# Kernel optimization log

Hardware: AMD Instinct MI355X
Metric: run time of the kernel (lower is better)

## Reference

```python
import jax, jax.numpy as jnp
import numpy as np

N, D, O, H, T, S, R, BN = 4096, 256, 256, 256, 512, 8, 4, 2  # nodes, in, out, hidden, text_len, adj_size, relations used, basis_num


def setup_inputs() -> dict:
    key = jax.random.key(0)
    ks = jax.random.split(key, 16)
    sc = 0.05
    return {
        "entity_embeddings": jax.random.normal(ks[0], (N, D), jnp.float32) * sc,
        "text_encodings": jax.random.normal(ks[1], (1, T, 2 * H), jnp.float32) * sc,
        "adj_to_use": jnp.arange(R, dtype=jnp.int32),
        "adj_masks": jax.random.randint(ks[2], (R, N, N), 0, 2, dtype=jnp.int32),
        "text_guids": jax.random.normal(ks[3], (S, 2 * H), jnp.float32) * sc,
        "graph_guids_1": jax.random.normal(ks[4], (S, D), jnp.float32) * sc,
        "graph_guids_2": jax.random.normal(ks[5], (S, D), jnp.float32) * sc,
        "guid_a": jax.random.normal(ks[6], (S,), jnp.float32),
        "basis_V": jax.random.normal(ks[7], (D, BN, O), jnp.float32) * sc,
        "basis_b": jax.random.normal(ks[8], (S, BN), jnp.float32) * sc,
        "W_1": jax.random.normal(ks[9], (2 * H, D), jnp.float32) * sc,
        "W_2": jax.random.normal(ks[10], (2 * H, D), jnp.float32) * sc,
        "ln_gamma": jnp.ones((O,), jnp.float32),
        "ln_beta": jnp.zeros((O,), jnp.float32),
    }


def reference(entity_embeddings, text_encodings, adj_to_use, adj_masks,
              text_guids, graph_guids_1, graph_guids_2, guid_a,
              basis_V, basis_b, W_1, W_2, ln_gamma, ln_beta):
    te = text_encodings[0]                                  # [T, 2H] (batch of 1)
    tg = text_guids[adj_to_use]                             # [R, 2H]
    # text attention: softmax over T, per relation
    att = jax.nn.softmax(te @ tg.T, axis=0)                 # [T, R]
    context = att.T @ te                                    # [R, 2H]
    c1 = context @ W_1                                      # [R, D]
    c2 = context @ W_2
    ga = jax.nn.sigmoid(guid_a[adj_to_use])[:, None]        # [R, 1]
    g1 = ga * graph_guids_1[adj_to_use] + (1.0 - ga) * c1   # [R, D]
    g2 = ga * graph_guids_2[adj_to_use] + (1.0 - ga) * c2
    s1 = entity_embeddings @ g1.T                           # [N, R]
    s2 = entity_embeddings @ g2.T
    # A[r,i,j] = s1[i,r] + s2[j,r], masked softmax over j
    A = s1.T[:, :, None] + s2.T[:, None, :]                 # [R, N, N]
    A = jnp.where(adj_masks == 1, A, jnp.float32(-1e10))
    A = jax.nn.softmax(A, axis=-1)
    fused = jnp.einsum('rij,jd->rid', A, entity_embeddings) # [R, N, D]
    # torch.cat over relations on last dim -> column index r*D + d
    fused_cat = jnp.transpose(fused, (1, 0, 2)).reshape(N, R * D)
    # torch.matmul([R,BN],[D,BN,O]) -> [D,R,O], then .view(R*D, O) (row index d*R + r)
    bb = basis_b[adj_to_use]                                # [R, BN]
    W = jnp.einsum('rb,dbo->dro', bb, basis_V).reshape(D * R, O)
    out = fused_cat @ W                                     # [N, O]
    mu = jnp.mean(out, axis=-1, keepdims=True)
    var = jnp.var(out, axis=-1, keepdims=True)
    out = (out - mu) / jnp.sqrt(var + 1e-5) * ln_gamma + ln_beta
    return jax.nn.relu(out)
```

## Files before the change

kernel.cpp:

```cpp
#include <hip/hip_runtime.h>
#include <hip/hip_bf16.h>


typedef unsigned short u16;
typedef short bf16x8 __attribute__((ext_vector_type(8)));
typedef float f32x4 __attribute__((ext_vector_type(4)));
typedef int   v4i   __attribute__((ext_vector_type(4)));
typedef unsigned int v2u __attribute__((ext_vector_type(2)));

#define G2_OFF    0
#define E2_OFF    4096
#define WRT_OFF   69632
#define FPT_OFF   593920
#define FUSED_OFF 9506816
#define CAN_OFF   26284032

#define C_ENT 0
#define C_TE  1048576
#define C_TG  1310720
#define C_GG2 1314816
#define C_GA  1316864
#define C_BV  1316872
#define C_BB  1447944
#define C_W2  1447960
#define C_GAM 1579032
#define C_BET 1579288

__device__ __forceinline__ float b2f(u16 u) {
    union { unsigned int i; float f; } v; v.i = ((unsigned int)u) << 16; return v.f;
}
__device__ __forceinline__ u16 f2b(float f) {
    union { float f; unsigned int i; } v; v.f = f;
    return (u16)((v.i + 0x7FFFu + ((v.i >> 16) & 1u)) >> 16);
}

__global__ __launch_bounds__(256) void k_cvt(
    const void* s0, const void* s1, const void* s2, const void* s3,
    const void* s4, const void* s5, const void* s6, const void* s7,
    const void* s8, const void* s9, const unsigned* __restrict__ graw,
    u16* __restrict__ dst)
{
    bool isbf = (graw[0] == 0x3F803F80u);
    const void* srcs[10] = {s0, s1, s2, s3, s4, s5, s6, s7, s8, s9};
    const int ns[10]     = {1048576, 262144, 4096, 2048, 8, 131072, 16, 131072, 256, 256};
    const int offs[10]   = {C_ENT, C_TE, C_TG, C_GG2, C_GA, C_BV, C_BB, C_W2, C_GAM, C_BET};
    const int bstart[11] = {0, 512, 640, 642, 643, 644, 708, 709, 773, 774, 775};
    int b = blockIdx.x, a = 0;
    while (b >= bstart[a + 1]) ++a;
    int rel = b - bstart[a];
    int n = ns[a];
    u16* d = dst + offs[a];
    int base = rel * 2048 + threadIdx.x;
    if (isbf) {
        const u16* s = (const u16*)srcs[a];
        for (int k = 0; k < 8; ++k) { int i = base + k * 256; if (i < n) d[i] = s[i]; }
    } else {
        const float* s = (const float*)srcs[a];
        for (int k = 0; k < 8; ++k) { int i = base + k * 256; if (i < n) d[i] = f2b(s[i]); }
    }
}

__global__ __launch_bounds__(1024) void k_pre(const u16* __restrict__ te,
                                              const int* __restrict__ adj,
                                              const u16* __restrict__ tguids,
                                              const u16* __restrict__ gg2,
                                              const u16* __restrict__ guida,
                                              const u16* __restrict__ W2,
                                              float* __restrict__ g2ws) {
    __shared__ float s_tg[4 * 512];
    __shared__ float s_att[512 * 4];
    __shared__ float s_red[512 * 4];
    __shared__ float s_ctx[4 * 512];
    __shared__ float s_part[1024 * 4];
    int tid = threadIdx.x;
    int a[4] = {adj[0], adj[1], adj[2], adj[3]};
    for (int idx = tid; idx < 2048; idx += 1024) {
        int r = idx >> 9, h = idx & 511;
        s_tg[r * 512 + h] = b2f(tguids[a[r] * 512 + h]);
    }
    __syncthreads();
    {
        int t = tid & 511, half = tid >> 9;
        int h0 = half * 256;
        float s0 = 0.f, s1 = 0.f, s2 = 0.f, s3 = 0.f;
        const u16* row = te + t * 512 + h0;
        for (int hb = 0; hb < 256; hb += 8) {
            bf16x8 v = *(const bf16x8*)(row + hb);
            #pragma unroll
            for (int k = 0; k < 8; ++k) {
                float tv = b2f((u16)v[k]);
                int h = h0 + hb + k;
                s0 += tv * s_tg[h];        s1 += tv * s_tg[512 + h];
                s2 += tv * s_tg[1024 + h]; s3 += tv * s_tg[1536 + h];
            }
        }
        s_part[tid * 4 + 0] = s0; s_part[tid * 4 + 1] = s1;
        s_part[tid * 4 + 2] = s2; s_part[tid * 4 + 3] = s3;
    }
    __syncthreads();
    if (tid < 512) {
        for (int r = 0; r < 4; ++r) {
            float s = s_part[tid * 4 + r] + s_part[(512 + tid) * 4 + r];
            s_att[tid * 4 + r] = s; s_red[tid * 4 + r] = s;
        }
    }
    __syncthreads();
    for (int st = 256; st > 0; st >>= 1) {
        if (tid < st) for (int r = 0; r < 4; ++r)
            s_red[tid * 4 + r] = fmaxf(s_red[tid * 4 + r], s_red[(tid + st) * 4 + r]);
        __syncthreads();
    }
    float mx[4]; for (int r = 0; r < 4; ++r) mx[r] = s_red[r];
    __syncthreads();
    if (tid < 512) for (int r = 0; r < 4; ++r) {
        float e = __expf(s_att[tid * 4 + r] - mx[r]);
        s_att[tid * 4 + r] = e; s_red[tid * 4 + r] = e;
    }
    __syncthreads();
    for (int st = 256; st > 0; st >>= 1) {
        if (tid < st) for (int r = 0; r < 4; ++r)
            s_red[tid * 4 + r] += s_red[(tid + st) * 4 + r];
        __syncthreads();
    }
    float dn[4]; for (int r = 0; r < 4; ++r) dn[r] = s_red[r];
    __syncthreads();
    if (tid < 512) for (int r = 0; r < 4; ++r) s_att[tid * 4 + r] /= dn[r];
    __syncthreads();
    {
        int u = tid >> 2, tq = tid & 3;
        int r = u >> 6, h0 = (u & 63) * 8;
        float acc[8] = {};
        int t0 = tq * 128;
        for (int t = t0; t < t0 + 128; ++t) {
            bf16x8 v = *(const bf16x8*)(te + t * 512 + h0);
            float at = s_att[t * 4 + r];
            #pragma unroll
            for (int k = 0; k < 8; ++k) acc[k] += at * b2f((u16)v[k]);
        }
        #pragma unroll
        for (int k = 0; k < 8; ++k) {
            acc[k] += __shfl_xor(acc[k], 1);
            acc[k] += __shfl_xor(acc[k], 2);
        }
        if (tq == 0) {
            #pragma unroll
            for (int k = 0; k < 8; ++k) s_ctx[r * 512 + h0 + k] = acc[k];
        }
    }
    __syncthreads();
    {
        int r = tid >> 8, d = tid & 255;
        float acc = 0.f;
        for (int h = 0; h < 512; ++h) acc += s_ctx[r * 512 + h] * b2f(W2[h * 256 + d]);
        float gav = 1.f / (1.f + expf(-b2f(guida[a[r]])));
        g2ws[r * 256 + d] = gav * b2f(gg2[a[r] * 256 + d]) + (1.f - gav) * acc;
    }
}

__global__ __launch_bounds__(256) void k_s2_wrt(const u16* __restrict__ entity,
                                                const int* __restrict__ adj,
                                                const u16* __restrict__ basisV,
                                                const u16* __restrict__ basisb,
                                                const float* __restrict__ g2ws,
                                                float* __restrict__ e2ws,
                                                u16* __restrict__ wrt) {
    int b = blockIdx.x, tid = threadIdx.x;
    if (b < 16) {
        __shared__ float sg2[1024];
        for (int i = tid; i < 1024; i += 256) sg2[i] = g2ws[i];
        __syncthreads();
        int j = b * 256 + tid;
        const u16* erow = entity + j * 256;
        float a0 = 0.f, a1 = 0.f, a2 = 0.f, a3 = 0.f;
        for (int d0 = 0; d0 < 256; d0 += 8) {
            bf16x8 v = *(const bf16x8*)(erow + d0);
            #pragma unroll
            for (int k = 0; k < 8; ++k) {
                float ev = b2f((u16)v[k]);
                a0 += ev * sg2[d0 + k];       a1 += ev * sg2[256 + d0 + k];
                a2 += ev * sg2[512 + d0 + k]; a3 += ev * sg2[768 + d0 + k];
            }
        }
        e2ws[j] = expf(a0); e2ws[4096 + j] = expf(a1);
        e2ws[8192 + j] = expf(a2); e2ws[12288 + j] = expf(a3);
    } else {
        int b2 = b - 16; int r = b2 >> 6;
        int c = (b2 & 63) * 4 + (tid >> 6);
        int dq = tid & 63;
        int dbase = dq * 4;
        int a[4] = {adj[0], adj[1], adj[2], adj[3]};
        for (int dd = 0; dd < 4; ++dd) {
            float w = 0.f;
            for (int bi = 0; bi < 2; ++bi)
                w += b2f(basisb[a[dd] * 2 + bi]) * b2f(basisV[((64 * r + dq) * 2 + bi) * 256 + c]);
            wrt[(r * 256 + c) * 256 + dbase + dd] = f2b(w);
        }
    }
}

__global__ __launch_bounds__(256) void k_fplus(const u16* __restrict__ entity,
                                               const u16* __restrict__ wrt,
                                               const float* __restrict__ e2ws,
                                               u16* __restrict__ fpt) {
    int b = blockIdx.x, tid = threadIdx.x;
    if (b < 256) {
        int r = b & 3, ct = (b >> 2) & 3, jt = b >> 4;
        int c0 = ct * 64, j0 = jt * 256;
        __shared__ __align__(16) u16 lw[64 * 264];
        const u16* wr = wrt + (r * 256 + c0) * 256;
        for (int k = 0; k < 8; ++k) {
            int ci = tid + k * 256; int row = ci >> 5, off = (ci & 31) * 8;
            *(v4i*)(&lw[row * 264 + off]) = *(const v4i*)(wr + row * 256 + off);
        }
        __syncthreads();
        int wave = tid >> 6, ln = tid & 15, q = (tid & 63) >> 4;
        f32x4 acc[4][4] = {};
        for (int ks = 0; ks < 8; ++ks) {
            bf16x8 afr[4], bfr[4];
            for (int mt = 0; mt < 4; ++mt)
                afr[mt] = *(const bf16x8*)(&lw[(mt * 16 + ln) * 264 + ks * 32 + q * 8]);
            for (int nt = 0; nt < 4; ++nt) {
                int j = j0 + (wave * 4 + nt) * 16 + ln;
                bfr[nt] = *(const bf16x8*)(entity + j * 256 + ks * 32 + q * 8);
            }
            for (int mt = 0; mt < 4; ++mt)
                for (int nt = 0; nt < 4; ++nt)
                    acc[mt][nt] = __builtin_amdgcn_mfma_f32_16x16x32_bf16(afr[mt], bfr[nt], acc[mt][nt], 0, 0, 0);
        }
        for (int nt = 0; nt < 4; ++nt) {
            int j = j0 + (wave * 4 + nt) * 16 + ln;
            float e2j = e2ws[r * 4096 + j];
            int kt = j >> 5, kk = j & 31;
            u16* dst = fpt + (((size_t)(r * 128 + kt)) * 272 << 5);
            for (int mt = 0; mt < 4; ++mt)
                for (int reg = 0; reg < 4; ++reg) {
                    int c = c0 + mt * 16 + q * 4 + reg;
                    dst[(c << 5) + kk] = f2b(acc[mt][nt][reg] * e2j);
                }
        }
    } else {
        int b2 = b - 256; int r = b2 >> 1, half = b2 & 1;
        const float* e2r = e2ws + r * 4096;
        for (int it = 0; it < 128; ++it) {
            int l = it * 256 + tid;
            int kk = l & 31;
            int c  = 256 + ((l >> 5) & 15);
            int kt = half * 64 + (l >> 9);
            fpt[(((size_t)(r * 128 + kt) * 272 + c) << 5) + kk] =
                (c == 256) ? f2b(e2r[kt * 32 + kk]) : (u16)0;
        }
    }
}

__global__ __launch_bounds__(512) void k_big(const int* __restrict__ masks,
                                             const u16* __restrict__ fpt,
                                             float* __restrict__ fused) {
    __shared__ __align__(16) u16 lm[2][64 * 40];
    __shared__ __align__(16) u16 lf[2][272 * 40];
    __shared__ float lden[64];
    int b = blockIdx.x, tid = threadIdx.x;
    int xcd = b & 7; int r = xcd & 3;
    int it = (b >> 3) + ((xcd >> 2) << 5);
    long i0 = (long)it * 64;
    const int* mbase = masks + ((long)r << 24) + i0 * 4096;
    const u16* fbase = fpt + (size_t)r * 128 * 272 * 32;
    int mrow = tid >> 3, mch = tid & 7;
    int wave = tid >> 6, lane = tid & 63, ln = lane & 15, q = lane >> 4;
    int mg = wave >> 2, ng = wave & 3;

    f32x4 acc[2][4] = {};
    f32x4 accD0 = {}, accD1 = {};

    struct Slot { v4i pm, f0, f1, f2; };
    Slot s0, s1, s2, s3;
    auto load_slot = [&](int kt, Slot& s) {
        s.pm = __builtin_nontemporal_load((const v4i*)(mbase + mrow * 4096 + kt * 32 + mch * 4));
        const u16* su = fbase + (size_t)kt * 8704;
        s.f0 = *(const v4i*)(su + tid * 8);
        s.f1 = *(const v4i*)(su + (tid + 512) * 8);
        if (tid < 64) s.f2 = *(const v4i*)(su + (tid + 1024) * 8);
    };
    auto stage = [&](int par, const Slot& s) {
        {
            unsigned m0 = (unsigned)s.pm.x * 0x3F80u, m1 = (unsigned)s.pm.y * 0x3F80u;
            unsigned m2 = (unsigned)s.pm.z * 0x3F80u, m3 = (unsigned)s.pm.w * 0x3F80u;
            v2u w; w.x = m0 | (m1 << 16); w.y = m2 | (m3 << 16);
            *(v2u*)(&lm[par][mrow * 40 + mch * 4]) = w;
        }
        u16* dst = &lf[par][0];
        *(v4i*)(dst + (tid >> 2) * 40 + (tid & 3) * 8) = s.f0;
        { int ci = tid + 512; *(v4i*)(dst + (ci >> 2) * 40 + (ci & 3) * 8) = s.f1; }
        if (tid < 64) { int ci = tid + 1024; *(v4i*)(dst + (ci >> 2) * 40 + (ci & 3) * 8) = s.f2; }
    };
    auto step = [&](int k, Slot& sM, Slot& sF) {
        const u16* msrc = &lm[k & 1][0];
        const u16* src  = &lf[k & 1][0];
        bf16x8 a0 = *(const bf16x8*)(msrc + (mg * 32 + ln) * 40 + q * 8);
        bf16x8 a1 = *(const bf16x8*)(msrc + (mg * 32 + 16 + ln) * 40 + q * 8);
        if (k + 1 < 128) stage((k + 1) & 1, sF);
        if (k + 4 < 128) load_slot(k + 4, sM);
        #pragma unroll
        for (int nt = 0; nt < 4; ++nt) {
            bf16x8 bf = *(const bf16x8*)(src + ((ng * 4 + nt) * 16 + ln) * 40 + q * 8);
            acc[0][nt] = __builtin_amdgcn_mfma_f32_16x16x32_bf16(a0, bf, acc[0][nt], 0, 0, 0);
            acc[1][nt] = __builtin_amdgcn_mfma_f32_16x16x32_bf16(a1, bf, acc[1][nt], 0, 0, 0);
        }
        if (ng == 3) {
            bf16x8 bf = *(const bf16x8*)(src + (256 + ln) * 40 + q * 8);
            accD0 = __builtin_amdgcn_mfma_f32_16x16x32_bf16(a0, bf, accD0, 0, 0, 0);
            accD1 = __builtin_amdgcn_mfma_f32_16x16x32_bf16(a1, bf, accD1, 0, 0, 0);
        }
        __syncthreads();
    };

    load_slot(0, s0);
    load_slot(1, s1);
    load_slot(2, s2);
    load_slot(3, s3);
    stage(0, s0);
    __syncthreads();
    #pragma unroll 1
    for (int kt = 0; kt < 128; kt += 4) {
        step(kt,     s0, s1);
        step(kt + 1, s1, s2);
        step(kt + 2, s2, s3);
        step(kt + 3, s3, s0);
    }

    if (ng == 3 && ln == 0) {
        #pragma unroll
        for (int reg = 0; reg < 4; ++reg) {
            lden[mg * 32 + q * 4 + reg]      = accD0[reg];
            lden[mg * 32 + 16 + q * 4 + reg] = accD1[reg];
        }
    }
    __syncthreads();
    float* fb = fused + ((long)r * 4096 + i0) * 256;
    #pragma unroll
    for (int mt = 0; mt < 2; ++mt) {
        float rd[4];
        #pragma unroll
        for (int reg = 0; reg < 4; ++reg) rd[reg] = 1.0f / lden[mg * 32 + mt * 16 + q * 4 + reg];
        #pragma unroll
        for (int nt = 0; nt < 4; ++nt) {
            int c = (ng * 4 + nt) * 16 + ln;
            #pragma unroll
            for (int reg = 0; reg < 4; ++reg) {
                int row = mg * 32 + mt * 16 + q * 4 + reg;
                __builtin_nontemporal_store(acc[mt][nt][reg] * rd[reg], fb + row * 256 + c);
            }
        }
    }
}

__global__ __launch_bounds__(256) void k_ln(const float* __restrict__ fused,
                                            const u16* __restrict__ gamma,
                                            const u16* __restrict__ beta,
                                            const unsigned* __restrict__ graw,
                                            void* __restrict__ outraw) {
    __shared__ float part[8];
    int i = blockIdx.x, o = threadIdx.x;
    float x = 0.f;
    for (int r = 0; r < 4; ++r)
        x += __builtin_nontemporal_load(fused + ((long)(r << 12) + i) * 256 + o);
    float s = x;
    #pragma unroll
    for (int st = 32; st > 0; st >>= 1) s += __shfl_xor(s, st);
    int w = o >> 6;
    if ((o & 63) == 0) part[w] = s;
    __syncthreads();
    float mu = (part[0] + part[1] + part[2] + part[3]) * (1.f / 256.f);
    float v = x - mu;
    float qv = v * v;
    #pragma unroll
    for (int st = 32; st > 0; st >>= 1) qv += __shfl_xor(qv, st);
    if ((o & 63) == 0) part[4 + w] = qv;
    __syncthreads();
    float var = (part[4] + part[5] + part[6] + part[7]) * (1.f / 256.f);
    float y = v * rsqrtf(var + 1e-5f) * b2f(gamma[o]) + b2f(beta[o]);
    float res = fmaxf(y, 0.f);
    bool isbf = (graw[0] == 0x3F803F80u);
    if (isbf) ((u16*)outraw)[i * 256 + o] = f2b(res);
    else      ((float*)outraw)[i * 256 + o] = res;
}

extern "C" void kernel_launch(void* const* d_in, const int* in_sizes, int n_in,
                              void* d_out, int out_size, void* d_ws, size_t ws_size,
                              hipStream_t stream) {
    const int* adj   = (const int*)d_in[2];
    const int* masks = (const int*)d_in[3];
    const unsigned* graw = (const unsigned*)d_in[12];
    char* ws = (char*)d_ws;
    float* g2ws = (float*)(ws + G2_OFF);
    float* e2ws = (float*)(ws + E2_OFF);
    u16*   wrt  = (u16*)(ws + WRT_OFF);
    u16*   fpt  = (u16*)(ws + FPT_OFF);
    float* fus  = (float*)(ws + FUSED_OFF);
    u16*   can  = (u16*)(ws + CAN_OFF);

    k_cvt<<<775, 256, 0, stream>>>(d_in[0], d_in[1], d_in[4], d_in[6], d_in[7],
                                   d_in[8], d_in[9], d_in[11], d_in[12], d_in[13],
                                   graw, can);
    const u16* entity = can + C_ENT;
    const u16* te     = can + C_TE;
    const u16* tguids = can + C_TG;
    const u16* gg2    = can + C_GG2;
    const u16* guida  = can + C_GA;
    const u16* basisV = can + C_BV;
    const u16* basisb = can + C_BB;
    const u16* W2     = can + C_W2;
    const u16* gamma  = can + C_GAM;
    const u16* beta   = can + C_BET;

    k_pre<<<1, 1024, 0, stream>>>(te, adj, tguids, gg2, guida, W2, g2ws);
    k_s2_wrt<<<272, 256, 0, stream>>>(entity, adj, basisV, basisb, g2ws, e2ws, wrt);
    k_fplus<<<264, 256, 0, stream>>>(entity, wrt, e2ws, fpt);
    k_big<<<256, 512, 0, stream>>>(masks, fpt, fus);
    k_ln<<<4096, 256, 0, stream>>>(fus, gamma, beta, graw, d_out);
}
```

Baseline: 545.5 us.

## Merge front-end kernels and fold exp(s2) into fplus to cut launches

Replaces the separate conversion, text-attention, and s2/basis-weight kernels with one k_front kernel. It converts only the entity table, builds the basis weights from raw inputs, and runs the attention/context/g2 block in a single 512-thread block. The exp(entity·g2) values are now recomputed inside k_fplus blocks instead of being staged through workspace, and the LN kernel reads gamma/beta raw. This removes two kernel launches and the conversion of unused tensors. In exchange, the single-block g2 path runs serially alongside the conversion blocks, and entity dot products are recomputed redundantly per block.

```diff
diff --git a/kernel.cpp b/kernel.cpp
--- a/kernel.cpp
+++ b/kernel.cpp
@@ -5,27 +5,16 @@
 typedef unsigned short u16;
 typedef short bf16x8 __attribute__((ext_vector_type(8)));
 typedef float f32x4 __attribute__((ext_vector_type(4)));
+typedef float f32x8 __attribute__((ext_vector_type(8)));
 typedef int   v4i   __attribute__((ext_vector_type(4)));
 typedef unsigned int v2u __attribute__((ext_vector_type(2)));
 
 #define G2_OFF    0
-#define E2_OFF    4096
 #define WRT_OFF   69632
 #define FPT_OFF   593920
 #define FUSED_OFF 9506816
 #define CAN_OFF   26284032
 
-#define C_ENT 0
-#define C_TE  1048576
-#define C_TG  1310720
-#define C_GG2 1314816
-#define C_GA  1316864
-#define C_BV  1316872
-#define C_BB  1447944
-#define C_W2  1447960
-#define C_GAM 1579032
-#define C_BET 1579288
-
 __device__ __forceinline__ float b2f(u16 u) {
     union { unsigned int i; float f; } v; v.i = ((unsigned int)u) << 16; return v.f;
 }
@@ -33,76 +22,89 @@
     union { float f; unsigned int i; } v; v.f = f;
     return (u16)((v.i + 0x7FFFu + ((v.i >> 16) & 1u)) >> 16);
 }
-
-__global__ __launch_bounds__(256) void k_cvt(
-    const void* s0, const void* s1, const void* s2, const void* s3,
-    const void* s4, const void* s5, const void* s6, const void* s7,
-    const void* s8, const void* s9, const unsigned* __restrict__ graw,
-    u16* __restrict__ dst)
+__device__ __forceinline__ float rawf(const void* p, bool isbf, int i) {
+    return isbf ? b2f(((const u16*)p)[i]) : ((const float*)p)[i];
+}
+__device__ __forceinline__ f32x8 raw8(const void* p, bool isbf, int i8) {
+    f32x8 o;
+    if (isbf) {
+        bf16x8 v = *(const bf16x8*)((const u16*)p + i8);
+        #pragma unroll
+        for (int k = 0; k < 8; ++k) o[k] = b2f((u16)v[k]);
+    } else {
+        const float* f = (const float*)p + i8;
+        float4 a = *(const float4*)f, b = *(const float4*)(f + 4);
+        o[0] = a.x; o[1] = a.y; o[2] = a.z; o[3] = a.w;
+        o[4] = b.x; o[5] = b.y; o[6] = b.z; o[7] = b.w;
+    }
+    return o;
+}
+
+__global__ __launch_bounds__(512) void k_front(
+    const void* __restrict__ ent_raw, const void* __restrict__ te_raw,
+    const int* __restrict__ adj, const void* __restrict__ tg_raw,
+    const void* __restrict__ gg2_raw, const void* __restrict__ ga_raw,
+    const void* __restrict__ bV_raw, const void* __restrict__ bb_raw,
+    const void* __restrict__ W2_raw, const unsigned* __restrict__ graw,
+    u16* __restrict__ ent_can, float* __restrict__ g2ws, u16* __restrict__ wrt)
 {
     bool isbf = (graw[0] == 0x3F803F80u);
-    const void* srcs[10] = {s0, s1, s2, s3, s4, s5, s6, s7, s8, s9};
-    const int ns[10]     = {1048576, 262144, 4096, 2048, 8, 131072, 16, 131072, 256, 256};
-    const int offs[10]   = {C_ENT, C_TE, C_TG, C_GG2, C_GA, C_BV, C_BB, C_W2, C_GAM, C_BET};
-    const int bstart[11] = {0, 512, 640, 642, 643, 644, 708, 709, 773, 774, 775};
-    int b = blockIdx.x, a = 0;
-    while (b >= bstart[a + 1]) ++a;
-    int rel = b - bstart[a];
-    int n = ns[a];
-    u16* d = dst + offs[a];
-    int base = rel * 2048 + threadIdx.x;
-    if (isbf) {
-        const u16* s = (const u16*)srcs[a];
-        for (int k = 0; k < 8; ++k) { int i = base + k * 256; if (i < n) d[i] = s[i]; }
-    } else {
-        const float* s = (const float*)srcs[a];
-        for (int k = 0; k < 8; ++k) { int i = base + k * 256; if (i < n) d[i] = f2b(s[i]); }
-    }
-}
-
-__global__ __launch_bounds__(1024) void k_pre(const u16* __restrict__ te,
-                                              const int* __restrict__ adj,
-                                              const u16* __restrict__ tguids,
-                                              const u16* __restrict__ gg2,
-                                              const u16* __restrict__ guida,
-                                              const u16* __restrict__ W2,
-                                              float* __restrict__ g2ws) {
+    int b = blockIdx.x, tid = threadIdx.x;
+    if (b < 256) {
+        int base = b * 4096 + tid;
+        if (isbf) {
+            const u16* s = (const u16*)ent_raw;
+            #pragma unroll
+            for (int k = 0; k < 8; ++k) { int i = base + k * 512; ent_can[i] = s[i]; }
+        } else {
+            const float* s = (const float*)ent_raw;
+            #pragma unroll
+            for (int k = 0; k < 8; ++k) { int i = base + k * 512; ent_can[i] = f2b(s[i]); }
+        }
+        return;
+    }
+    if (b < 384) {
+        int b2 = b - 256;
+        int r = b2 >> 5, cq = b2 & 31;
+        int c = cq * 8 + (tid >> 6);
+        int dq = tid & 63;
+        int a[4] = {adj[0], adj[1], adj[2], adj[3]};
+        #pragma unroll
+        for (int dd = 0; dd < 4; ++dd) {
+            float w = 0.f;
+            #pragma unroll
+            for (int bi = 0; bi < 2; ++bi)
+                w += rawf(bb_raw, isbf, a[dd] * 2 + bi) *
+                     rawf(bV_raw, isbf, ((64 * r + dq) * 2 + bi) * 256 + c);
+            wrt[(r * 256 + c) * 256 + dq * 4 + dd] = f2b(w);
+        }
+        return;
+    }
     __shared__ float s_tg[4 * 512];
     __shared__ float s_att[512 * 4];
     __shared__ float s_red[512 * 4];
     __shared__ float s_ctx[4 * 512];
-    __shared__ float s_part[1024 * 4];
-    int tid = threadIdx.x;
     int a[4] = {adj[0], adj[1], adj[2], adj[3]};
-    for (int idx = tid; idx < 2048; idx += 1024) {
+    for (int idx = tid; idx < 2048; idx += 512) {
         int r = idx >> 9, h = idx & 511;
-        s_tg[r * 512 + h] = b2f(tguids[a[r] * 512 + h]);
+        s_tg[r * 512 + h] = rawf(tg_raw, isbf, a[r] * 512 + h);
     }
     __syncthreads();
     {
-        int t = tid & 511, half = tid >> 9;
-        int h0 = half * 256;
         float s0 = 0.f, s1 = 0.f, s2 = 0.f, s3 = 0.f;
-        const u16* row = te + t * 512 + h0;
-        for (int hb = 0; hb < 256; hb += 8) {
-            bf16x8 v = *(const bf16x8*)(row + hb);
+        for (int hb = 0; hb < 512; hb += 8) {
+            f32x8 v = raw8(te_raw, isbf, tid * 512 + hb);
             #pragma unroll
             for (int k = 0; k < 8; ++k) {
-                float tv = b2f((u16)v[k]);
-                int h = h0 + hb + k;
+                float tv = v[k]; int h = hb + k;
                 s0 += tv * s_tg[h];        s1 += tv * s_tg[512 + h];
                 s2 += tv * s_tg[1024 + h]; s3 += tv * s_tg[1536 + h];
             }
         }
-        s_part[tid * 4 + 0] = s0; s_part[tid * 4 + 1] = s1;
-        s_part[tid * 4 + 2] = s2; s_part[tid * 4 + 3] = s3;
-    }
-    __syncthreads();
-    if (tid < 512) {
-        for (int r = 0; r < 4; ++r) {
-            float s = s_part[tid * 4 + r] + s_part[(512 + tid) * 4 + r];
-            s_att[tid * 4 + r] = s; s_red[tid * 4 + r] = s;
-        }
+        s_att[tid * 4 + 0] = s0; s_red[tid * 4 + 0] = s0;
+        s_att[tid * 4 + 1] = s1; s_red[tid * 4 + 1] = s1;
+        s_att[tid * 4 + 2] = s2; s_red[tid * 4 + 2] = s2;
+        s_att[tid * 4 + 3] = s3; s_red[tid * 4 + 3] = s3;
     }
     __syncthreads();
     for (int st = 256; st > 0; st >>= 1) {
@@ -112,7 +114,7 @@
     }
     float mx[4]; for (int r = 0; r < 4; ++r) mx[r] = s_red[r];
     __syncthreads();
-    if (tid < 512) for (int r = 0; r < 4; ++r) {
+    for (int r = 0; r < 4; ++r) {
         float e = __expf(s_att[tid * 4 + r] - mx[r]);
         s_att[tid * 4 + r] = e; s_red[tid * 4 + r] = e;
     }
@@ -124,24 +126,21 @@
     }
     float dn[4]; for (int r = 0; r < 4; ++r) dn[r] = s_red[r];
     __syncthreads();
-    if (tid < 512) for (int r = 0; r < 4; ++r) s_att[tid * 4 + r] /= dn[r];
+    for (int r = 0; r < 4; ++r) s_att[tid * 4 + r] /= dn[r];
     __syncthreads();
     {
-        int u = tid >> 2, tq = tid & 3;
+        int u = tid >> 1, tq = tid & 1;
         int r = u >> 6, h0 = (u & 63) * 8;
         float acc[8] = {};
-        int t0 = tq * 128;
-        for (int t = t0; t < t0 + 128; ++t) {
-            bf16x8 v = *(const bf16x8*)(te + t * 512 + h0);
+        int t0 = tq * 256;
+        for (int t = t0; t < t0 + 256; ++t) {
+            f32x8 v = raw8(te_raw, isbf, t * 512 + h0);
             float at = s_att[t * 4 + r];
             #pragma unroll
-            for (int k = 0; k < 8; ++k) acc[k] += at * b2f((u16)v[k]);
-        }
-        #pragma unroll
-        for (int k = 0; k < 8; ++k) {
-            acc[k] += __shfl_xor(acc[k], 1);
-            acc[k] += __shfl_xor(acc[k], 2);
-        }
+            for (int k = 0; k < 8; ++k) acc[k] += at * v[k];
+        }
+        #pragma unroll
+        for (int k = 0; k < 8; ++k) acc[k] += __shfl_xor(acc[k], 1);
         if (tq == 0) {
             #pragma unroll
             for (int k = 0; k < 8; ++k) s_ctx[r * 512 + h0 + k] = acc[k];
@@ -149,68 +148,45 @@
     }
     __syncthreads();
     {
-        int r = tid >> 8, d = tid & 255;
-        float acc = 0.f;
-        for (int h = 0; h < 512; ++h) acc += s_ctx[r * 512 + h] * b2f(W2[h * 256 + d]);
-        float gav = 1.f / (1.f + expf(-b2f(guida[a[r]])));
-        g2ws[r * 256 + d] = gav * b2f(gg2[a[r] * 256 + d]) + (1.f - gav) * acc;
-    }
-}
-
-__global__ __launch_bounds__(256) void k_s2_wrt(const u16* __restrict__ entity,
-                                                const int* __restrict__ adj,
-                                                const u16* __restrict__ basisV,
-                                                const u16* __restrict__ basisb,
-                                                const float* __restrict__ g2ws,
-                                                float* __restrict__ e2ws,
-                                                u16* __restrict__ wrt) {
-    int b = blockIdx.x, tid = threadIdx.x;
-    if (b < 16) {
-        __shared__ float sg2[1024];
-        for (int i = tid; i < 1024; i += 256) sg2[i] = g2ws[i];
-        __syncthreads();
-        int j = b * 256 + tid;
-        const u16* erow = entity + j * 256;
-        float a0 = 0.f, a1 = 0.f, a2 = 0.f, a3 = 0.f;
-        for (int d0 = 0; d0 < 256; d0 += 8) {
-            bf16x8 v = *(const bf16x8*)(erow + d0);
-            #pragma unroll
-            for (int k = 0; k < 8; ++k) {
-                float ev = b2f((u16)v[k]);
-                a0 += ev * sg2[d0 + k];       a1 += ev * sg2[256 + d0 + k];
-                a2 += ev * sg2[512 + d0 + k]; a3 += ev * sg2[768 + d0 + k];
-            }
-        }
-        e2ws[j] = expf(a0); e2ws[4096 + j] = expf(a1);
-        e2ws[8192 + j] = expf(a2); e2ws[12288 + j] = expf(a3);
-    } else {
-        int b2 = b - 16; int r = b2 >> 6;
-        int c = (b2 & 63) * 4 + (tid >> 6);
-        int dq = tid & 63;
-        int dbase = dq * 4;
-        int a[4] = {adj[0], adj[1], adj[2], adj[3]};
-        for (int dd = 0; dd < 4; ++dd) {
-            float w = 0.f;
-            for (int bi = 0; bi < 2; ++bi)
-                w += b2f(basisb[a[dd] * 2 + bi]) * b2f(basisV[((64 * r + dq) * 2 + bi) * 256 + c]);
-            wrt[(r * 256 + c) * 256 + dbase + dd] = f2b(w);
+        for (int rep = 0; rep < 2; ++rep) {
+            int o = tid + rep * 512;
+            int r = o >> 8, d = o & 255;
+            float acc = 0.f;
+            for (int h = 0; h < 512; ++h)
+                acc += s_ctx[r * 512 + h] * rawf(W2_raw, isbf, h * 256 + d);
+            float gav = 1.f / (1.f + expf(-rawf(ga_raw, isbf, a[r])));
+            g2ws[r * 256 + d] = gav * rawf(gg2_raw, isbf, a[r] * 256 + d) + (1.f - gav) * acc;
         }
     }
 }
 
 __global__ __launch_bounds__(256) void k_fplus(const u16* __restrict__ entity,
                                                const u16* __restrict__ wrt,
-                                               const float* __restrict__ e2ws,
+                                               const float* __restrict__ g2ws,
                                                u16* __restrict__ fpt) {
     int b = blockIdx.x, tid = threadIdx.x;
     if (b < 256) {
         int r = b & 3, ct = (b >> 2) & 3, jt = b >> 4;
         int c0 = ct * 64, j0 = jt * 256;
         __shared__ __align__(16) u16 lw[64 * 264];
+        __shared__ float sg2[256];
+        __shared__ float sE[256];
         const u16* wr = wrt + (r * 256 + c0) * 256;
         for (int k = 0; k < 8; ++k) {
             int ci = tid + k * 256; int row = ci >> 5, off = (ci & 31) * 8;
             *(v4i*)(&lw[row * 264 + off]) = *(const v4i*)(wr + row * 256 + off);
+        }
+        sg2[tid] = g2ws[r * 256 + tid];
+        __syncthreads();
+        {
+            const u16* erow = entity + (j0 + tid) * 256;
+            float acc = 0.f;
+            for (int d0 = 0; d0 < 256; d0 += 8) {
+                bf16x8 v = *(const bf16x8*)(erow + d0);
+                #pragma unroll
+                for (int k = 0; k < 8; ++k) acc += b2f((u16)v[k]) * sg2[d0 + k];
+            }
+            sE[tid] = expf(acc);
         }
         __syncthreads();
         int wave = tid >> 6, ln = tid & 15, q = (tid & 63) >> 4;
@@ -229,7 +205,7 @@
         }
         for (int nt = 0; nt < 4; ++nt) {
             int j = j0 + (wave * 4 + nt) * 16 + ln;
-            float e2j = e2ws[r * 4096 + j];
+            float e2j = sE[(wave * 4 + nt) * 16 + ln];
             int kt = j >> 5, kk = j & 31;
             u16* dst = fpt + (((size_t)(r * 128 + kt)) * 272 << 5);
             for (int mt = 0; mt < 4; ++mt)
@@ -240,14 +216,29 @@
         }
     } else {
         int b2 = b - 256; int r = b2 >> 1, half = b2 & 1;
-        const float* e2r = e2ws + r * 4096;
+        __shared__ float sg2z[256];
+        __shared__ float sE2[2048];
+        sg2z[tid] = g2ws[r * 256 + tid];
+        __syncthreads();
+        for (int s = 0; s < 8; ++s) {
+            int jj = half * 2048 + s * 256 + tid;
+            const u16* erow = entity + jj * 256;
+            float acc = 0.f;
+            for (int d0 = 0; d0 < 256; d0 += 8) {
+                bf16x8 v = *(const bf16x8*)(erow + d0);
+                #pragma unroll
+                for (int k = 0; k < 8; ++k) acc += b2f((u16)v[k]) * sg2z[d0 + k];
+            }
+            sE2[s * 256 + tid] = expf(acc);
+        }
+        __syncthreads();
         for (int it = 0; it < 128; ++it) {
             int l = it * 256 + tid;
             int kk = l & 31;
             int c  = 256 + ((l >> 5) & 15);
             int kt = half * 64 + (l >> 9);
             fpt[(((size_t)(r * 128 + kt) * 272 + c) << 5) + kk] =
-                (c == 256) ? f2b(e2r[kt * 32 + kk]) : (u16)0;
+                (c == 256) ? f2b(sE2[kt * 32 + kk - half * 2048]) : (u16)0;
         }
     }
 }
@@ -354,12 +345,13 @@
 }
 
 __global__ __launch_bounds__(256) void k_ln(const float* __restrict__ fused,
-                                            const u16* __restrict__ gamma,
-                                            const u16* __restrict__ beta,
+                                            const void* __restrict__ gamma_raw,
+                                            const void* __restrict__ beta_raw,
                                             const unsigned* __restrict__ graw,
                                             void* __restrict__ outraw) {
     __shared__ float part[8];
     int i = blockIdx.x, o = threadIdx.x;
+    bool isbf = (graw[0] == 0x3F803F80u);
     float x = 0.f;
     for (int r = 0; r < 4; ++r)
         x += __builtin_nontemporal_load(fused + ((long)(r << 12) + i) * 256 + o);
@@ -377,9 +369,8 @@
     if ((o & 63) == 0) part[4 + w] = qv;
     __syncthreads();
     float var = (part[4] + part[5] + part[6] + part[7]) * (1.f / 256.f);
-    float y = v * rsqrtf(var + 1e-5f) * b2f(gamma[o]) + b2f(beta[o]);
+    float y = v * rsqrtf(var + 1e-5f) * rawf(gamma_raw, isbf, o) + rawf(beta_raw, isbf, o);
     float res = fmaxf(y, 0.f);
-    bool isbf = (graw[0] == 0x3F803F80u);
     if (isbf) ((u16*)outraw)[i * 256 + o] = f2b(res);
     else      ((float*)outraw)[i * 256 + o] = res;
 }
@@ -392,29 +383,15 @@
     const unsigned* graw = (const unsigned*)d_in[12];
     char* ws = (char*)d_ws;
     float* g2ws = (float*)(ws + G2_OFF);
-    float* e2ws = (float*)(ws + E2_OFF);
     u16*   wrt  = (u16*)(ws + WRT_OFF);
     u16*   fpt  = (u16*)(ws + FPT_OFF);
     float* fus  = (float*)(ws + FUSED_OFF);
-    u16*   can  = (u16*)(ws + CAN_OFF);
-
-    k_cvt<<<775, 256, 0, stream>>>(d_in[0], d_in[1], d_in[4], d_in[6], d_in[7],
-                                   d_in[8], d_in[9], d_in[11], d_in[12], d_in[13],
-                                   graw, can);
-    const u16* entity = can + C_ENT;
-    const u16* te     = can + C_TE;
-    const u16* tguids = can + C_TG;
-    const u16* gg2    = can + C_GG2;
-    const u16* guida  = can + C_GA;
-    const u16* basisV = can + C_BV;
-    const u16* basisb = can + C_BB;
-    const u16* W2     = can + C_W2;
-    const u16* gamma  = can + C_GAM;
-    const u16* beta   = can + C_BET;
-
-    k_pre<<<1, 1024, 0, stream>>>(te, adj, tguids, gg2, guida, W2, g2ws);
-    k_s2_wrt<<<272, 256, 0, stream>>>(entity, adj, basisV, basisb, g2ws, e2ws, wrt);
-    k_fplus<<<264, 256, 0, stream>>>(entity, wrt, e2ws, fpt);
+    u16*   ent  = (u16*)(ws + CAN_OFF);
+
+    k_front<<<385, 512, 0, stream>>>(d_in[0], d_in[1], adj, d_in[4], d_in[6],
+                                     d_in[7], d_in[8], d_in[9], d_in[11],
+                                     graw, ent, g2ws, wrt);
+    k_fplus<<<264, 256, 0, stream>>>(ent, wrt, g2ws, fpt);
     k_big<<<256, 512, 0, stream>>>(masks, fpt, fus);
-    k_ln<<<4096, 256, 0, stream>>>(fus, gamma, beta, graw, d_out);
-}
+    k_ln<<<4096, 256, 0, stream>>>(fus, d_in[12], d_in[13], graw, d_out);
+}
```

New measurement: 679.7 us. 24.6% more time.
